# Kernel optimization log

Hardware: AMD Instinct MI355X
Metric: run time of the kernel (lower is better)

## Reference

```python
import jax, jax.numpy as jnp
import numpy as np

N, M = 100000, 12
A, E = 128, 64
BN_EPS = 1e-5

def batchnorm(x, gamma, beta):
    # training-mode BN over leading dim, biased variance (torch default)
    mean = jnp.mean(x, axis=0)
    var = jnp.var(x, axis=0)
    return (x - mean) * jax.lax.rsqrt(var + BN_EPS) * gamma + beta

def setup_inputs() -> dict:
    key = jax.random.key(0)
    ks = jax.random.split(key, 9)
    s_in = 1.0 / np.sqrt(2 * A + E)
    s_skip = 1.0 / np.sqrt(A)
    return {
        "atom_in_fea": jax.random.normal(ks[0], (N, A), jnp.float32),
        "nbr_fea": jax.random.normal(ks[1], (N, M, E), jnp.float32),
        "nbr_fea_idx": jax.random.randint(ks[2], (N, M), 0, N),
        "W_full": jax.random.uniform(ks[3], (2 * A + E, 2 * A), jnp.float32, -s_in, s_in),
        "b_full": jax.random.uniform(ks[4], (2 * A,), jnp.float32, -s_in, s_in),
        "gamma1": jnp.ones((2 * A,), jnp.float32),
        "beta1": jnp.zeros((2 * A,), jnp.float32),
        "gamma2": jnp.ones((A,), jnp.float32),
        "beta2": jnp.zeros((A,), jnp.float32),
        "W_skip": jax.random.uniform(ks[5], (A, A), jnp.float32, -s_skip, s_skip),
        "b_skip": jax.random.uniform(ks[6], (A,), jnp.float32, -s_skip, s_skip),
    }

def reference(atom_in_fea, nbr_fea, nbr_fea_idx, W_full, b_full,
              gamma1, beta1, gamma2, beta2, W_skip, b_skip):
    atom_nbr_fea = atom_in_fea[nbr_fea_idx]                      # [N,M,A] gather
    atom_self_fea = jnp.broadcast_to(atom_in_fea[:, None, :], (N, M, A))
    total = jnp.concatenate([atom_self_fea, atom_nbr_fea, nbr_fea], axis=2)  # [N,M,2A+E]
    gated = jnp.einsum('nmf,fg->nmg', total, W_full) + b_full    # [N,M,2A]
    gated = batchnorm(gated.reshape(-1, 2 * A), gamma1, beta1).reshape(N, M, 2 * A)
    nbr_filter, nbr_core = gated[..., :A], gated[..., A:]
    nbr_sumed = jnp.sum(jax.nn.sigmoid(nbr_filter) * jax.nn.softplus(nbr_core), axis=1)  # [N,A]
    nbr_sumed = batchnorm(nbr_sumed, gamma2, beta2)
    skip_val = atom_in_fea @ W_skip + b_skip
    return jax.nn.softplus(skip_val + nbr_sumed)
```

## Files before the change

### kernel.cpp

```cpp
#include <hip/hip_runtime.h>
#include <stdint.h>

#define N_ATOM 100000
#define M_NBR 12
#define A_FEA 128
#define E_FEA 64
#define KDIM 320
#define GDIM 256
#define ROWS (N_ATOM*M_NBR)
#define BN_EPS 1e-5f

typedef unsigned short u16;
typedef unsigned int u32;
typedef __attribute__((ext_vector_type(8))) short short8;
typedef __attribute__((ext_vector_type(4))) float f32x4;

#define S_BN1SUM 0
#define S_BN1SSQ 256
#define S_S1 512
#define S_T1 768
#define S_BN2SUM 1024
#define S_BN2SSQ 1152
#define S_S2 1280
#define S_T2 1408
#define STATS_F32 1536

#define WPQ_OFF 0
#define W3T_OFF 131072
#define WSK_OFF 163840
#define STATS_OFF 196608
#define P_OFF 202752
#define PQ_BYTES ((size_t)N_ATOM*256*2)
#define Q_OFF (P_OFF + PQ_BYTES)
#define NEED_FAST3 (P_OFF + 2*PQ_BYTES)

__device__ __forceinline__ u16 f2bf(float x) {
    union { float f; u32 u; } v; v.f = x;
    u32 r = v.u + 0x7FFFu + ((v.u >> 16) & 1u);
    return (u16)(r >> 16);
}
__device__ __forceinline__ float bflo(u32 x) { return __uint_as_float(x << 16); }
__device__ __forceinline__ float bfhi(u32 x) { return __uint_as_float(x & 0xFFFF0000u); }
__device__ __forceinline__ float softplus_f(float x) {
    return fmaxf(x, 0.f) + __logf(1.f + __expf(-fabsf(x)));
}
__device__ __forceinline__ float sigmoid_f(float x) {
    return 1.f / (1.f + __expf(-x));
}

__global__ void zero_stats(float* __restrict__ stats) {
    int t = threadIdx.x;
    stats[t] = 0.f;
    stats[256 + t] = 0.f;
    stats[1024 + t] = 0.f;
}

__global__ void finalize1(const float* __restrict__ g1, const float* __restrict__ b1,
                          float* __restrict__ stats) {
    int c = threadIdx.x;
    const float inv_cnt = 1.f / (float)ROWS;
    float mean = stats[S_BN1SUM + c] * inv_cnt;
    float var  = stats[S_BN1SSQ + c] * inv_cnt - mean * mean;
    float iv = rsqrtf(var + BN_EPS);
    float s = g1[c] * iv;
    stats[S_S1 + c] = s;
    stats[S_T1 + c] = fmaf(-mean, s, b1[c]);
}

__global__ void finalize2(const float* __restrict__ g2, const float* __restrict__ b2,
                          float* __restrict__ stats) {
    int c = threadIdx.x;
    const float inv_cnt = 1.f / (float)N_ATOM;
    float mean = stats[S_BN2SUM + c] * inv_cnt;
    float var  = stats[S_BN2SSQ + c] * inv_cnt - mean * mean;
    float iv = rsqrtf(var + BN_EPS);
    float s = g2[c] * iv;
    stats[S_S2 + c] = s;
    stats[S_T2 + c] = fmaf(-mean, s, b2[c]);
}

__global__ void prep_pack2(const float* __restrict__ Wfull,
                           const float* __restrict__ Wskip,
                           u16* __restrict__ wpq, u16* __restrict__ w3t,
                           u16* __restrict__ wsk) {
    int tid = blockIdx.x * blockDim.x + threadIdx.x;
    int l = tid & 63, fr = l & 15, fq = l >> 4;
    if (tid < 8192) {
        int ct = (tid >> 6) & 31;
        int kt = tid >> 11;
        int c = ct * 16 + fr;
        int k0 = kt * 32 + fq * 8;
        u16 tmp[8];
        #pragma unroll
        for (int i = 0; i < 8; ++i) {
            int kk = k0 + i;
            float v = (c < 256) ? Wfull[kk * GDIM + c]
                                : Wfull[(128 + kk) * GDIM + (c - 256)];
            tmp[i] = f2bf(v);
        }
        uint4 pk;
        pk.x = (u32)tmp[0] | ((u32)tmp[1] << 16);
        pk.y = (u32)tmp[2] | ((u32)tmp[3] << 16);
        pk.z = (u32)tmp[4] | ((u32)tmp[5] << 16);
        pk.w = (u32)tmp[6] | ((u32)tmp[7] << 16);
        *reinterpret_cast<uint4*>(&wpq[tid * 8]) = pk;
    } else if (tid < 10240) {
        int t2 = tid - 8192;
        int frag = t2 >> 6;
        int rt16 = frag & 15, kt = frag >> 4;
        int gcol = rt16 * 16 + fr;
        int k0 = kt * 32 + fq * 8;
        u16 tmp[8];
        #pragma unroll
        for (int i = 0; i < 8; ++i) tmp[i] = f2bf(Wfull[(256 + k0 + i) * GDIM + gcol]);
        uint4 pk;
        pk.x = (u32)tmp[0] | ((u32)tmp[1] << 16);
        pk.y = (u32)tmp[2] | ((u32)tmp[3] << 16);
        pk.z = (u32)tmp[4] | ((u32)tmp[5] << 16);
        pk.w = (u32)tmp[6] | ((u32)tmp[7] << 16);
        *reinterpret_cast<uint4*>(&w3t[t2 * 8]) = pk;
    } else if (tid < 12288) {
        int t3 = tid - 10240;
        int ct = (t3 >> 6) & 7;
        int kt = t3 >> 9;
        int c = ct * 16 + fr;
        int k0 = kt * 32 + fq * 8;
        u16 tmp[8];
        #pragma unroll
        for (int i = 0; i < 8; ++i) tmp[i] = f2bf(Wskip[(k0 + i) * A_FEA + c]);
        uint4 pk;
        pk.x = (u32)tmp[0] | ((u32)tmp[1] << 16);
        pk.y = (u32)tmp[2] | ((u32)tmp[3] << 16);
        pk.z = (u32)tmp[4] | ((u32)tmp[5] << 16);
        pk.w = (u32)tmp[6] | ((u32)tmp[7] << 16);
        *reinterpret_cast<uint4*>(&wsk[t3 * 8]) = pk;
    }
}

__launch_bounds__(256)
__global__ void pq_kernel(const float* __restrict__ atom_in,
                          const u16* __restrict__ wpq,
                          u16* __restrict__ Pb, u16* __restrict__ Qb) {
    __shared__ u16 al[64 * 130];
    const int t = threadIdx.x;
    const int w = t >> 6, l = t & 63, fr = l & 15, fq = l >> 4;
    const int n0 = blockIdx.x * 64;

    #pragma unroll
    for (int it = 0; it < 4; ++it) {
        int c = t + it * 256;
        int row = c >> 4, seg = c & 15;
        int n = n0 + row;
        uint4 pk = {0u, 0u, 0u, 0u};
        if (n < N_ATOM) {
            const float* src = atom_in + (size_t)n * A_FEA + seg * 8;
            float4 x0 = *reinterpret_cast<const float4*>(src);
            float4 x1 = *reinterpret_cast<const float4*>(src + 4);
            pk.x = (u32)f2bf(x0.x) | ((u32)f2bf(x0.y) << 16);
            pk.y = (u32)f2bf(x0.z) | ((u32)f2bf(x0.w) << 16);
            pk.z = (u32)f2bf(x1.x) | ((u32)f2bf(x1.y) << 16);
            pk.w = (u32)f2bf(x1.z) | ((u32)f2bf(x1.w) << 16);
        }
        *reinterpret_cast<uint4*>(&al[row * 130 + seg * 8]) = pk;
    }
    __syncthreads();

    f32x4 acc[4][8];
    #pragma unroll
    for (int rt = 0; rt < 4; ++rt)
        #pragma unroll
        for (int p = 0; p < 8; ++p)
            acc[rt][p] = (f32x4){0.f,0.f,0.f,0.f};

    for (int kt = 0; kt < 4; ++kt) {
        short8 af[4], bf[8];
        #pragma unroll
        for (int rt = 0; rt < 4; ++rt)
            af[rt] = *reinterpret_cast<const short8*>(
                &al[(rt * 16 + fr) * 130 + kt * 32 + fq * 8]);
        #pragma unroll
        for (int p = 0; p < 8; ++p)
            bf[p] = *reinterpret_cast<const short8*>(
                &wpq[((kt * 32 + w * 8 + p) * 64 + l) * 8]);
        #pragma unroll
        for (int rt = 0; rt < 4; ++rt)
            #pragma unroll
            for (int p = 0; p < 8; ++p)
                acc[rt][p] = __builtin_amdgcn_mfma_f32_16x16x32_bf16(
                    af[rt], bf[p], acc[rt][p], 0, 0, 0);
    }

    #pragma unroll
    for (int p = 0; p < 8; ++p) {
        int col = w * 128 + p * 16 + fr;
        u16* dst = (col < 256) ? Pb : Qb;
        int cc = (col < 256) ? col : (col - 256);
        #pragma unroll
        for (int rt = 0; rt < 4; ++rt)
            #pragma unroll
            for (int j = 0; j < 4; ++j) {
                int n = n0 + rt * 16 + fq * 4 + j;
                if (n < N_ATOM) dst[(size_t)n * 256 + cc] = f2bf(acc[rt][p][j]);
            }
    }
}

#define NTILES_E (ROWS/96)
#define GRID_E 2500
#define EPAD 66
#define PPAD2 264
#define ACT2 132
#define E_SH6 (96*EPAD*2)
#define P_SH6 E_SH6
#define I_SH6 (E_SH6 + 8*PPAD2*2)
#define SH6_M1 17280
#define SH6_M2 (96*ACT2*4)

template<int MODE>
__launch_bounds__(512, 2)
__global__ void estage6(const float* __restrict__ nbr_fea,
                        const int* __restrict__ nbr_idx,
                        const u16* __restrict__ w3t,
                        const u16* __restrict__ Pb,
                        const u16* __restrict__ Qb,
                        float* __restrict__ stats,
                        float* __restrict__ out_ns) {
    constexpr int SHB = (MODE == 1) ? SH6_M1 : SH6_M2;
    __shared__ __align__(16) unsigned char shraw[SHB];
    u16* e_lds = (u16*)shraw;
    u16* p_lds = (u16*)(shraw + P_SH6);
    int* idx_lds = (int*)(shraw + I_SH6);
    float* act = (float*)shraw;
    float* red = (float*)shraw;

    const int t = threadIdx.x;
    const int w = t >> 6, l = t & 63, fr = l & 15, fq = l >> 4;
    const int gbase0 = w * 16 + fq * 4;

    short8 aw[2][2];
    #pragma unroll
    for (int kt = 0; kt < 2; ++kt)
        #pragma unroll
        for (int rt = 0; rt < 2; ++rt)
            aw[kt][rt] = *reinterpret_cast<const short8*>(
                &w3t[(((kt * 16) + w + rt * 8) * 64 + l) * 8]);

    float s1v[2][4], t1v[2][4];
    if (MODE == 2) {
        #pragma unroll
        for (int rt = 0; rt < 2; ++rt)
            #pragma unroll
            for (int j = 0; j < 4; ++j) {
                int col = gbase0 + rt * 128 + j;
                s1v[rt][j] = stats[S_S1 + col];
                t1v[rt][j] = stats[S_T1 + col];
            }
    }
    float ls[2][4] = {{0,0,0,0},{0,0,0,0}}, lq[2][4] = {{0,0,0,0},{0,0,0,0}};
    float bsum = 0.f, bssq = 0.f;

    for (int tile = blockIdx.x; tile < NTILES_E; tile += GRID_E) {
        const int r0 = tile * 96;
        const int n0a = tile * 8;

        __syncthreads();

        #pragma unroll
        for (int i = 0; i < 2; ++i) {
            int o = t + i * 512;
            if (o < 768) {
                int row = o >> 3, seg = o & 7;
                const float* src = nbr_fea + (size_t)(r0 + row) * E_FEA + seg * 8;
                float4 x0 = *reinterpret_cast<const float4*>(src);
                float4 x1 = *reinterpret_cast<const float4*>(src + 4);
                uint4 pk;
                pk.x = (u32)f2bf(x0.x) | ((u32)f2bf(x0.y) << 16);
                pk.y = (u32)f2bf(x0.z) | ((u32)f2bf(x0.w) << 16);
                pk.z = (u32)f2bf(x1.x) | ((u32)f2bf(x1.y) << 16);
                pk.w = (u32)f2bf(x1.z) | ((u32)f2bf(x1.w) << 16);
                *reinterpret_cast<uint4*>(&e_lds[row * EPAD + seg * 8]) = pk;
            }
        }
        if (t < 256) {
            int row = t >> 5, seg = t & 31;
            *reinterpret_cast<uint4*>(&p_lds[row * PPAD2 + seg * 8]) =
                *reinterpret_cast<const uint4*>(&Pb[(size_t)(n0a + row) * 256 + seg * 8]);
        } else if (t >= 416) {
            int e = t - 416;
            idx_lds[e] = nbr_idx[r0 + e];
        }
        __syncthreads();

        uint2 qv0r[6], qv1r[6];
        #pragma unroll
        for (int ct = 0; ct < 6; ++ct) {
            int edge = ct * 16 + fr;
            int jr = idx_lds[edge];
            const u16* qb = Qb + (size_t)jr * 256;
            qv0r[ct] = *reinterpret_cast<const uint2*>(qb + gbase0);
            qv1r[ct] = *reinterpret_cast<const uint2*>(qb + gbase0 + 128);
        }

        f32x4 acc[2][6];
        #pragma unroll
        for (int rt = 0; rt < 2; ++rt)
            #pragma unroll
            for (int ct = 0; ct < 6; ++ct)
                acc[rt][ct] = (f32x4){0.f,0.f,0.f,0.f};
        #pragma unroll
        for (int kt = 0; kt < 2; ++kt) {
            short8 bf[6];
            #pragma unroll
            for (int ct = 0; ct < 6; ++ct)
                bf[ct] = *reinterpret_cast<const short8*>(
                    &e_lds[(ct * 16 + fr) * EPAD + kt * 32 + fq * 8]);
            #pragma unroll
            for (int rt = 0; rt < 2; ++rt)
                #pragma unroll
                for (int ct = 0; ct < 6; ++ct)
                    acc[rt][ct] = __builtin_amdgcn_mfma_f32_16x16x32_bf16(
                        aw[kt][rt], bf[ct], acc[rt][ct], 0, 0, 0);
        }

        if (MODE == 1) {
            #pragma unroll
            for (int ct = 0; ct < 6; ++ct) {
                int edge = ct * 16 + fr;
                int atom = (edge * 171) >> 11;
                uint2 qv0 = qv0r[ct], qv1 = qv1r[ct];
                uint2 pv0 = *reinterpret_cast<const uint2*>(&p_lds[atom * PPAD2 + gbase0]);
                uint2 pv1 = *reinterpret_cast<const uint2*>(&p_lds[atom * PPAD2 + gbase0 + 128]);
                float g;
                g = acc[0][ct][0] + bflo(qv0.x) + bflo(pv0.x); ls[0][0] += g; lq[0][0] = fmaf(g,g,lq[0][0]);
                g = acc[0][ct][1] + bfhi(qv0.x) + bfhi(pv0.x); ls[0][1] += g; lq[0][1] = fmaf(g,g,lq[0][1]);
                g = acc[0][ct][2] + bflo(qv0.y) + bflo(pv0.y); ls[0][2] += g; lq[0][2] = fmaf(g,g,lq[0][2]);
                g = acc[0][ct][3] + bfhi(qv0.y) + bfhi(pv0.y); ls[0][3] += g; lq[0][3] = fmaf(g,g,lq[0][3]);
                g = acc[1][ct][0] + bflo(qv1.x) + bflo(pv1.x); ls[1][0] += g; lq[1][0] = fmaf(g,g,lq[1][0]);
                g = acc[1][ct][1] + bfhi(qv1.x) + bfhi(pv1.x); ls[1][1] += g; lq[1][1] = fmaf(g,g,lq[1][1]);
                g = acc[1][ct][2] + bflo(qv1.y) + bflo(pv1.y); ls[1][2] += g; lq[1][2] = fmaf(g,g,lq[1][2]);
                g = acc[1][ct][3] + bfhi(qv1.y) + bfhi(pv1.y); ls[1][3] += g; lq[1][3] = fmaf(g,g,lq[1][3]);
            }
        } else {
            float ar[6][4];
            #pragma unroll
            for (int ct = 0; ct < 6; ++ct) {
                int edge = ct * 16 + fr;
                int atom = (edge * 171) >> 11;
                uint2 qv0 = qv0r[ct], qv1 = qv1r[ct];
                uint2 pv0 = *reinterpret_cast<const uint2*>(&p_lds[atom * PPAD2 + gbase0]);
                uint2 pv1 = *reinterpret_cast<const uint2*>(&p_lds[atom * PPAD2 + gbase0 + 128]);
                float gf, gc;
                gf = acc[0][ct][0] + bflo(qv0.x) + bflo(pv0.x);
                gc = acc[1][ct][0] + bflo(qv1.x) + bflo(pv1.x);
                ar[ct][0] = sigmoid_f(fmaf(gf, s1v[0][0], t1v[0][0])) * softplus_f(fmaf(gc, s1v[1][0], t1v[1][0]));
                gf = acc[0][ct][1] + bfhi(qv0.x) + bfhi(pv0.x);
                gc = acc[1][ct][1] + bfhi(qv1.x) + bfhi(pv1.x);
                ar[ct][1] = sigmoid_f(fmaf(gf, s1v[0][1], t1v[0][1])) * softplus_f(fmaf(gc, s1v[1][1], t1v[1][1]));
                gf = acc[0][ct][2] + bflo(qv0.y) + bflo(pv0.y);
                gc = acc[1][ct][2] + bflo(qv1.y) + bflo(pv1.y);
                ar[ct][2] = sigmoid_f(fmaf(gf, s1v[0][2], t1v[0][2])) * softplus_f(fmaf(gc, s1v[1][2], t1v[1][2]));
                gf = acc[0][ct][3] + bfhi(qv0.y) + bfhi(pv0.y);
                gc = acc[1][ct][3] + bfhi(qv1.y) + bfhi(pv1.y);
                ar[ct][3] = sigmoid_f(fmaf(gf, s1v[0][3], t1v[0][3])) * softplus_f(fmaf(gc, s1v[1][3], t1v[1][3]));
            }
            __syncthreads();
            #pragma unroll
            for (int ct = 0; ct < 6; ++ct) {
                int edge = ct * 16 + fr;
                float4 f4 = make_float4(ar[ct][0], ar[ct][1], ar[ct][2], ar[ct][3]);
                *reinterpret_cast<float4*>(&act[edge * ACT2 + gbase0]) = f4;
            }
            __syncthreads();
            #pragma unroll
            for (int i = 0; i < 2; ++i) {
                int o = i * 512 + t;
                int a = o >> 7;
                int c = t & 127;
                float S = 0.f;
                #pragma unroll
                for (int mm = 0; mm < 12; ++mm)
                    S += act[(a * 12 + mm) * ACT2 + c];
                out_ns[(size_t)(n0a + a) * A_FEA + c] = S;
                bsum += S;
                bssq = fmaf(S, S, bssq);
            }
        }
    }

    if (MODE == 1) {
        #pragma unroll
        for (int rt = 0; rt < 2; ++rt)
            #pragma unroll
            for (int j = 0; j < 4; ++j) {
                float s = ls[rt][j], q = lq[rt][j];
                s += __shfl_xor(s, 1, 64);  s += __shfl_xor(s, 2, 64);
                s += __shfl_xor(s, 4, 64);  s += __shfl_xor(s, 8, 64);
                q += __shfl_xor(q, 1, 64);  q += __shfl_xor(q, 2, 64);
                q += __shfl_xor(q, 4, 64);  q += __shfl_xor(q, 8, 64);
                if (fr == 0) {
                    int col = gbase0 + rt * 128 + j;
                    atomicAdd(&stats[S_BN1SUM + col], s);
                    atomicAdd(&stats[S_BN1SSQ + col], q);
                }
            }
    } else {
        __syncthreads();
        if (t >= 128) {
            red[(t - 128) * 2]     = bsum;
            red[(t - 128) * 2 + 1] = bssq;
        }
        __syncthreads();
        if (t < 128) {
            bsum += red[t * 2]     + red[(128 + t) * 2]     + red[(256 + t) * 2];
            bssq += red[t * 2 + 1] + red[(128 + t) * 2 + 1] + red[(256 + t) * 2 + 1];
            atomicAdd(&stats[S_BN2SUM + t], bsum);
            atomicAdd(&stats[S_BN2SSQ + t], bssq);
        }
    }
}

#define BM5 64
__launch_bounds__(256, 2)
__global__ void skip_kernel(const float* __restrict__ atom_in,
                            const u16* __restrict__ wsf,
                            const float* __restrict__ b_skip,
                            const float* __restrict__ stats,
                            float* __restrict__ out) {
    __shared__ u16 a5[BM5 * 136];
    const int t = threadIdx.x;
    const int w = t >> 6, l = t & 63, fr = l & 15, fq = l >> 4;
    const int n0 = blockIdx.x * BM5;

    #pragma unroll
    for (int it = 0; it < 4; ++it) {
        int c = t + it * 256;
        int row = c >> 4, seg = c & 15;
        int n = n0 + row;
        uint4 pk = {0u, 0u, 0u, 0u};
        if (n < N_ATOM) {
            const float* src = atom_in + (size_t)n * A_FEA + seg * 8;
            float4 x0 = *reinterpret_cast<const float4*>(src);
            float4 x1 = *reinterpret_cast<const float4*>(src + 4);
            pk.x = (u32)f2bf(x0.x) | ((u32)f2bf(x0.y) << 16);
            pk.y = (u32)f2bf(x0.z) | ((u32)f2bf(x0.w) << 16);
            pk.z = (u32)f2bf(x1.x) | ((u32)f2bf(x1.y) << 16);
            pk.w = (u32)f2bf(x1.z) | ((u32)f2bf(x1.w) << 16);
        }
        *reinterpret_cast<uint4*>(&a5[row * 136 + seg * 8]) = pk;
    }
    __syncthreads();

    f32x4 acc[4][2];
    #pragma unroll
    for (int rt = 0; rt < 4; ++rt) {
        acc[rt][0] = (f32x4){0.f,0.f,0.f,0.f};
        acc[rt][1] = (f32x4){0.f,0.f,0.f,0.f};
    }
    for (int kt = 0; kt < 4; ++kt) {
        short8 af[4], bf[2];
        #pragma unroll
        for (int rt = 0; rt < 4; ++rt)
            af[rt] = *reinterpret_cast<const short8*>(
                &a5[(rt * 16 + fr) * 136 + kt * 32 + fq * 8]);
        #pragma unroll
        for (int p = 0; p < 2; ++p)
            bf[p] = *reinterpret_cast<const short8*>(
                &wsf[((kt * 8 + 2 * w + p) * 64 + l) * 8]);
        #pragma unroll
        for (int rt = 0; rt < 4; ++rt)
            #pragma unroll
            for (int p = 0; p < 2; ++p)
                acc[rt][p] = __builtin_amdgcn_mfma_f32_16x16x32_bf16(
                    af[rt], bf[p], acc[rt][p], 0, 0, 0);
    }

    #pragma unroll
    for (int p = 0; p < 2; ++p) {
        int col = w * 32 + p * 16 + fr;
        float bs = b_skip[col];
        float s2 = stats[S_S2 + col];
        float t2 = stats[S_T2 + col];
        #pragma unroll
        for (int rt = 0; rt < 4; ++rt)
            #pragma unroll
            for (int j = 0; j < 4; ++j) {
                int n = n0 + rt * 16 + fq * 4 + j;
                if (n < N_ATOM) {
                    size_t o = (size_t)n * A_FEA + col;
                    float S = out[o];
                    out[o] = softplus_f(acc[rt][p][j] + bs + fmaf(S, s2, t2));
                }
            }
    }
}

#define BM 96
#define NTILES (ROWS/BM)
#define GRID_P 2500
#define TPB 256
#define APAD 328
#define ACTPAD 132

__global__ void prep_pack_slow(const float* __restrict__ Wfull,
                               const float* __restrict__ Wskip,
                               u16* __restrict__ wf, u16* __restrict__ wsf) {
    int tid = blockIdx.x * blockDim.x + threadIdx.x;
    if (tid < 10240) {
        int l = tid & 63;
        int ct = (tid >> 6) & 15;
        int kt = tid >> 10;
        int fr = l & 15, fq = l >> 4;
        int col = ct * 16 + fr;
        int k0 = kt * 32 + fq * 8;
        u16 tmp[8];
        #pragma unroll
        for (int i = 0; i < 8; ++i) tmp[i] = f2bf(Wfull[(k0 + i) * GDIM + col]);
        uint4 pk;
        pk.x = (u32)tmp[0] | ((u32)tmp[1] << 16);
        pk.y = (u32)tmp[2] | ((u32)tmp[3] << 16);
        pk.z = (u32)tmp[4] | ((u32)tmp[5] << 16);
        pk.w = (u32)tmp[6] | ((u32)tmp[7] << 16);
        *reinterpret_cast<uint4*>(&wf[tid * 8]) = pk;
    } else if (tid < 12288) {
        int t2 = tid - 10240;
        int l = t2 & 63;
        int ct = (t2 >> 6) & 7;
        int kt = t2 >> 9;
        int fr = l & 15, fq = l >> 4;
        int col = ct * 16 + fr;
        int k0 = kt * 32 + fq * 8;
        u16 tmp[8];
        #pragma unroll
        for (int i = 0; i < 8; ++i) tmp[i] = f2bf(Wskip[(k0 + i) * A_FEA + col]);
        uint4 pk;
        pk.x = (u32)tmp[0] | ((u32)tmp[1] << 16);
        pk.y = (u32)tmp[2] | ((u32)tmp[3] << 16);
        pk.z = (u32)tmp[4] | ((u32)tmp[5] << 16);
        pk.w = (u32)tmp[6] | ((u32)tmp[7] << 16);
        *reinterpret_cast<uint4*>(&wsf[t2 * 8]) = pk;
    }
}

template<int PASS>
__launch_bounds__(TPB, 2)
__global__ void pass_kernel(const float* __restrict__ atom_in,
                            const float* __restrict__ nbr_fea,
                            const int* __restrict__ nbr_idx,
                            const u16* __restrict__ wf,
                            float* __restrict__ stats,
                            float* __restrict__ out_ns) {
    __shared__ union {
        u16 a[BM * APAD];
        float act[BM * ACTPAD];
    } sh;

    const int t = threadIdx.x;
    const int w = t >> 6, l = t & 63, fr = l & 15, fq = l >> 4;
    const int ct0 = 2 * w;

    int colp[4];
    colp[0] = ct0 * 16 + fr;
    colp[1] = colp[0] + 16;
    colp[2] = colp[0] + 128;
    colp[3] = colp[1] + 128;

    float s1v[4], t1v[4];
    if (PASS == 2) {
        #pragma unroll
        for (int p = 0; p < 4; ++p) {
            s1v[p] = stats[S_S1 + colp[p]];
            t1v[p] = stats[S_T1 + colp[p]];
        }
    }
    float ls[4] = {0.f,0.f,0.f,0.f}, lq[4] = {0.f,0.f,0.f,0.f};
    float bsum = 0.f, bssq = 0.f;

    for (int tile = blockIdx.x; tile < NTILES; tile += GRID_P) {
        const int n0 = tile * 8;

        __syncthreads();
        for (int it = 0; it < 15; ++it) {
            int c = t + it * TPB;
            int row = c / 40;
            int seg = c - row * 40;
            int an = row / 12;
            int m  = row - an * 12;
            int na = n0 + an;
            const float* src;
            if (seg < 16) {
                src = atom_in + (size_t)na * A_FEA + seg * 8;
            } else if (seg < 32) {
                int j = nbr_idx[na * M_NBR + m];
                src = atom_in + (size_t)j * A_FEA + (seg - 16) * 8;
            } else {
                src = nbr_fea + ((size_t)na * M_NBR + m) * E_FEA + (seg - 32) * 8;
            }
            float4 x0 = *reinterpret_cast<const float4*>(src);
            float4 x1 = *reinterpret_cast<const float4*>(src + 4);
            uint4 pk;
            pk.x = (u32)f2bf(x0.x) | ((u32)f2bf(x0.y) << 16);
            pk.y = (u32)f2bf(x0.z) | ((u32)f2bf(x0.w) << 16);
            pk.z = (u32)f2bf(x1.x) | ((u32)f2bf(x1.y) << 16);
            pk.w = (u32)f2bf(x1.z) | ((u32)f2bf(x1.w) << 16);
            *reinterpret_cast<uint4*>(&sh.a[row * APAD + seg * 8]) = pk;
        }
        __syncthreads();

        f32x4 acc[6][4];
        #pragma unroll
        for (int rt = 0; rt < 6; ++rt)
            #pragma unroll
            for (int p = 0; p < 4; ++p)
                acc[rt][p] = (f32x4){0.f,0.f,0.f,0.f};

        for (int kt = 0; kt < 10; ++kt) {
            short8 af[6], bf[4];
            #pragma unroll
            for (int rt = 0; rt < 6; ++rt)
                af[rt] = *reinterpret_cast<const short8*>(
                    &sh.a[(rt * 16 + fr) * APAD + kt * 32 + fq * 8]);
            #pragma unroll
            for (int p = 0; p < 4; ++p) {
                int ct = (p < 2) ? (ct0 + p) : (ct0 + 8 + (p - 2));
                bf[p] = *reinterpret_cast<const short8*>(
                    &wf[((kt * 16 + ct) * 64 + l) * 8]);
            }
            #pragma unroll
            for (int rt = 0; rt < 6; ++rt)
                #pragma unroll
                for (int p = 0; p < 4; ++p)
                    acc[rt][p] = __builtin_amdgcn_mfma_f32_16x16x32_bf16(
                        af[rt], bf[p], acc[rt][p], 0, 0, 0);
        }

        if (PASS == 1) {
            #pragma unroll
            for (int p = 0; p < 4; ++p)
                #pragma unroll
                for (int rt = 0; rt < 6; ++rt)
                    #pragma unroll
                    for (int j = 0; j < 4; ++j) {
                        float v = acc[rt][p][j];
                        ls[p] += v;
                        lq[p] = fmaf(v, v, lq[p]);
                    }
        } else {
            __syncthreads();
            #pragma unroll
            for (int rt = 0; rt < 6; ++rt)
                #pragma unroll
                for (int p = 0; p < 2; ++p)
                    #pragma unroll
                    for (int j = 0; j < 4; ++j) {
                        float gf = fmaf(acc[rt][p][j],     s1v[p],     t1v[p]);
                        float gc = fmaf(acc[rt][2 + p][j], s1v[2 + p], t1v[2 + p]);
                        float a = sigmoid_f(gf) * softplus_f(gc);
                        int row = rt * 16 + fq * 4 + j;
                        int colact = ct0 * 16 + p * 16 + fr;
                        sh.act[row * ACTPAD + colact] = a;
                    }
            __syncthreads();
            #pragma unroll
            for (int i = 0; i < 4; ++i) {
                int o = i * TPB + t;
                int a = o >> 7;
                int c = o & 127;
                float S = 0.f;
                #pragma unroll
                for (int mm = 0; mm < 12; ++mm)
                    S += sh.act[(a * 12 + mm) * ACTPAD + c];
                out_ns[(size_t)(n0 + a) * A_FEA + c] = S;
                bsum += S;
                bssq = fmaf(S, S, bssq);
            }
        }
    }

    if (PASS == 1) {
        #pragma unroll
        for (int p = 0; p < 4; ++p) {
            float s = ls[p], q = lq[p];
            s += __shfl_xor(s, 16, 64);
            s += __shfl_xor(s, 32, 64);
            q += __shfl_xor(q, 16, 64);
            q += __shfl_xor(q, 32, 64);
            if (fq == 0) {
                atomicAdd(&stats[S_BN1SUM + colp[p]], s);
                atomicAdd(&stats[S_BN1SSQ + colp[p]], q);
            }
        }
    } else {
        __syncthreads();
        if (t >= 128) {
            sh.act[(t - 128) * 2]     = bsum;
            sh.act[(t - 128) * 2 + 1] = bssq;
        }
        __syncthreads();
        if (t < 128) {
            bsum += sh.act[t * 2];
            bssq += sh.act[t * 2 + 1];
            atomicAdd(&stats[S_BN2SUM + t], bsum);
            atomicAdd(&stats[S_BN2SSQ + t], bssq);
        }
    }
}

extern "C" void kernel_launch(void* const* d_in, const int* in_sizes, int n_in,
                              void* d_out, int out_size, void* d_ws, size_t ws_size,
                              hipStream_t stream) {
    (void)in_sizes; (void)n_in; (void)out_size;
    const float* atom_in = (const float*)d_in[0];
    const float* nbr_fea = (const float*)d_in[1];
    const int*   nbr_idx = (const int*)d_in[2];
    const float* Wfull   = (const float*)d_in[3];
    const float* g1      = (const float*)d_in[5];
    const float* b1      = (const float*)d_in[6];
    const float* g2      = (const float*)d_in[7];
    const float* b2      = (const float*)d_in[8];
    const float* Wsk     = (const float*)d_in[9];
    const float* bsk     = (const float*)d_in[10];
    float* out = (float*)d_out;

    float* stats = (float*)((char*)d_ws + STATS_OFF);
    u16* wskf = (u16*)((char*)d_ws + WSK_OFF);

    if (ws_size >= NEED_FAST3) {
        u16* wpq = (u16*)d_ws;
        u16* w3t = (u16*)((char*)d_ws + W3T_OFF);
        u16* Pb  = (u16*)((char*)d_ws + P_OFF);
        u16* Qb  = (u16*)((char*)d_ws + Q_OFF);

        zero_stats<<<1, 256, 0, stream>>>(stats);
        prep_pack2<<<48, 256, 0, stream>>>(Wfull, Wsk, wpq, w3t, wskf);
        pq_kernel<<<(N_ATOM + 63) / 64, 256, 0, stream>>>(atom_in, wpq, Pb, Qb);
        estage6<1><<<GRID_E, 512, 0, stream>>>(nbr_fea, nbr_idx, w3t, Pb, Qb, stats, out);
        finalize1<<<1, 256, 0, stream>>>(g1, b1, stats);
        estage6<2><<<GRID_E, 512, 0, stream>>>(nbr_fea, nbr_idx, w3t, Pb, Qb, stats, out);
        finalize2<<<1, 128, 0, stream>>>(g2, b2, stats);
        skip_kernel<<<(N_ATOM + BM5 - 1) / BM5, 256, 0, stream>>>(atom_in, wskf, bsk, stats, out);
    } else {
        u16* wf = (u16*)d_ws;
        zero_stats<<<1, 256, 0, stream>>>(stats);
        prep_pack_slow<<<48, 256, 0, stream>>>(Wfull, Wsk, wf, wskf);
        pass_kernel<1><<<GRID_P, TPB, 0, stream>>>(atom_in, nbr_fea, nbr_idx, wf, stats, out);
        finalize1<<<1, 256, 0, stream>>>(g1, b1, stats);
        pass_kernel<2><<<GRID_P, TPB, 0, stream>>>(atom_in, nbr_fea, nbr_idx, wf, stats, out);
        finalize2<<<1, 128, 0, stream>>>(g2, b2, stats);
        skip_kernel<<<(N_ATOM + BM5 - 1) / BM5, 256, 0, stream>>>(atom_in, wskf, bsk, stats, out);
    }
}
```

Baseline: 981.2 us.

## Materialize gated activations in bf16 instead of recomputing GEMM in second pass

Replaces the two-pass recompute scheme (running the edge GEMM twice, once for BN1 stats and once for the activation) with a single GEMM pass that writes the pre-BN gated values as bf16 to workspace, followed by a streaming apply kernel that normalizes, applies sigmoid*softplus, sums over neighbors and accumulates BN2 stats. This removes the second nbr_fea read, gather and MFMA pass at the cost of writing and rereading roughly 600 MB of bf16 intermediate. It also adds bf16 rounding of the pre-BN values and needs a larger workspace, falling back to the old path otherwise.

Result: faster. 841.4 us (-14.3%).

```diff
diff --git a/kernel.cpp b/kernel.cpp
--- a/kernel.cpp
+++ b/kernel.cpp
@@ -33,6 +33,9 @@
 #define PQ_BYTES ((size_t)N_ATOM*256*2)
 #define Q_OFF (P_OFF + PQ_BYTES)
 #define NEED_FAST3 (P_OFF + 2*PQ_BYTES)
+#define GATED_OFF NEED_FAST3
+#define GATED_BYTES ((size_t)ROWS*256*2)
+#define NEED_FASTW (GATED_OFF + GATED_BYTES)
 
 __device__ __forceinline__ u16 f2bf(float x) {
     union { float f; u32 u; } v; v.f = x;
@@ -209,10 +212,206 @@
 #define GRID_E 2500
 #define EPAD 66
 #define PPAD2 264
-#define ACT2 132
 #define E_SH6 (96*EPAD*2)
 #define P_SH6 E_SH6
 #define I_SH6 (E_SH6 + 8*PPAD2*2)
+#define SH7 17280
+
+__launch_bounds__(512, 2)
+__global__ void estage7(const float* __restrict__ nbr_fea,
+                        const int* __restrict__ nbr_idx,
+                        const u16* __restrict__ w3t,
+                        const u16* __restrict__ Pb,
+                        const u16* __restrict__ Qb,
+                        float* __restrict__ stats,
+                        u16* __restrict__ gated) {
+    __shared__ __align__(16) unsigned char shraw[SH7];
+    u16* e_lds = (u16*)shraw;
+    u16* p_lds = (u16*)(shraw + P_SH6);
+    int* idx_lds = (int*)(shraw + I_SH6);
+
+    const int t = threadIdx.x;
+    const int w = t >> 6, l = t & 63, fr = l & 15, fq = l >> 4;
+    const int gbase0 = w * 16 + fq * 4;
+
+    short8 aw[2][2];
+    #pragma unroll
+    for (int kt = 0; kt < 2; ++kt)
+        #pragma unroll
+        for (int rt = 0; rt < 2; ++rt)
+            aw[kt][rt] = *reinterpret_cast<const short8*>(
+                &w3t[(((kt * 16) + w + rt * 8) * 64 + l) * 8]);
+
+    float ls[2][4] = {{0,0,0,0},{0,0,0,0}}, lq[2][4] = {{0,0,0,0},{0,0,0,0}};
+
+    for (int tile = blockIdx.x; tile < NTILES_E; tile += GRID_E) {
+        const int r0 = tile * 96;
+        const int n0a = tile * 8;
+
+        __syncthreads();
+
+        #pragma unroll
+        for (int i = 0; i < 2; ++i) {
+            int o = t + i * 512;
+            if (o < 768) {
+                int row = o >> 3, seg = o & 7;
+                const float* src = nbr_fea + (size_t)(r0 + row) * E_FEA + seg * 8;
+                float4 x0 = *reinterpret_cast<const float4*>(src);
+                float4 x1 = *reinterpret_cast<const float4*>(src + 4);
+                uint4 pk;
+                pk.x = (u32)f2bf(x0.x) | ((u32)f2bf(x0.y) << 16);
+                pk.y = (u32)f2bf(x0.z) | ((u32)f2bf(x0.w) << 16);
+                pk.z = (u32)f2bf(x1.x) | ((u32)f2bf(x1.y) << 16);
+                pk.w = (u32)f2bf(x1.z) | ((u32)f2bf(x1.w) << 16);
+                *reinterpret_cast<uint4*>(&e_lds[row * EPAD + seg * 8]) = pk;
+            }
+        }
+        if (t < 256) {
+            int row = t >> 5, seg = t & 31;
+            *reinterpret_cast<uint4*>(&p_lds[row * PPAD2 + seg * 8]) =
+                *reinterpret_cast<const uint4*>(&Pb[(size_t)(n0a + row) * 256 + seg * 8]);
+        } else if (t >= 416) {
+            int e = t - 416;
+            idx_lds[e] = nbr_idx[r0 + e];
+        }
+        __syncthreads();
+
+        uint2 qv0r[6], qv1r[6];
+        #pragma unroll
+        for (int ct = 0; ct < 6; ++ct) {
+            int edge = ct * 16 + fr;
+            int jr = idx_lds[edge];
+            const u16* qb = Qb + (size_t)jr * 256;
+            qv0r[ct] = *reinterpret_cast<const uint2*>(qb + gbase0);
+            qv1r[ct] = *reinterpret_cast<const uint2*>(qb + gbase0 + 128);
+        }
+
+        f32x4 acc[2][6];
+        #pragma unroll
+        for (int rt = 0; rt < 2; ++rt)
+            #pragma unroll
+            for (int ct = 0; ct < 6; ++ct)
+                acc[rt][ct] = (f32x4){0.f,0.f,0.f,0.f};
+        #pragma unroll
+        for (int kt = 0; kt < 2; ++kt) {
+            short8 bf[6];
+            #pragma unroll
+            for (int ct = 0; ct < 6; ++ct)
+                bf[ct] = *reinterpret_cast<const short8*>(
+                    &e_lds[(ct * 16 + fr) * EPAD + kt * 32 + fq * 8]);
+            #pragma unroll
+            for (int rt = 0; rt < 2; ++rt)
+                #pragma unroll
+                for (int ct = 0; ct < 6; ++ct)
+                    acc[rt][ct] = __builtin_amdgcn_mfma_f32_16x16x32_bf16(
+                        aw[kt][rt], bf[ct], acc[rt][ct], 0, 0, 0);
+        }
+
+        #pragma unroll
+        for (int ct = 0; ct < 6; ++ct) {
+            int edge = ct * 16 + fr;
+            int atom = (edge * 171) >> 11;
+            uint2 qv0 = qv0r[ct], qv1 = qv1r[ct];
+            uint2 pv0 = *reinterpret_cast<const uint2*>(&p_lds[atom * PPAD2 + gbase0]);
+            uint2 pv1 = *reinterpret_cast<const uint2*>(&p_lds[atom * PPAD2 + gbase0 + 128]);
+            float g00 = acc[0][ct][0] + bflo(qv0.x) + bflo(pv0.x);
+            float g01 = acc[0][ct][1] + bfhi(qv0.x) + bfhi(pv0.x);
+            float g02 = acc[0][ct][2] + bflo(qv0.y) + bflo(pv0.y);
+            float g03 = acc[0][ct][3] + bfhi(qv0.y) + bfhi(pv0.y);
+            float g10 = acc[1][ct][0] + bflo(qv1.x) + bflo(pv1.x);
+            float g11 = acc[1][ct][1] + bfhi(qv1.x) + bfhi(pv1.x);
+            float g12 = acc[1][ct][2] + bflo(qv1.y) + bflo(pv1.y);
+            float g13 = acc[1][ct][3] + bfhi(qv1.y) + bfhi(pv1.y);
+            ls[0][0] += g00; lq[0][0] = fmaf(g00,g00,lq[0][0]);
+            ls[0][1] += g01; lq[0][1] = fmaf(g01,g01,lq[0][1]);
+            ls[0][2] += g02; lq[0][2] = fmaf(g02,g02,lq[0][2]);
+            ls[0][3] += g03; lq[0][3] = fmaf(g03,g03,lq[0][3]);
+            ls[1][0] += g10; lq[1][0] = fmaf(g10,g10,lq[1][0]);
+            ls[1][1] += g11; lq[1][1] = fmaf(g11,g11,lq[1][1]);
+            ls[1][2] += g12; lq[1][2] = fmaf(g12,g12,lq[1][2]);
+            ls[1][3] += g13; lq[1][3] = fmaf(g13,g13,lq[1][3]);
+            size_t grow = (size_t)(r0 + edge) * 256;
+            uint2 w0, w1;
+            w0.x = (u32)f2bf(g00) | ((u32)f2bf(g01) << 16);
+            w0.y = (u32)f2bf(g02) | ((u32)f2bf(g03) << 16);
+            w1.x = (u32)f2bf(g10) | ((u32)f2bf(g11) << 16);
+            w1.y = (u32)f2bf(g12) | ((u32)f2bf(g13) << 16);
+            *reinterpret_cast<uint2*>(&gated[grow + gbase0]) = w0;
+            *reinterpret_cast<uint2*>(&gated[grow + gbase0 + 128]) = w1;
+        }
+    }
+
+    #pragma unroll
+    for (int rt = 0; rt < 2; ++rt)
+        #pragma unroll
+        for (int j = 0; j < 4; ++j) {
+            float s = ls[rt][j], q = lq[rt][j];
+            s += __shfl_xor(s, 1, 64);  s += __shfl_xor(s, 2, 64);
+            s += __shfl_xor(s, 4, 64);  s += __shfl_xor(s, 8, 64);
+            q += __shfl_xor(q, 1, 64);  q += __shfl_xor(q, 2, 64);
+            q += __shfl_xor(q, 4, 64);  q += __shfl_xor(q, 8, 64);
+            if (fr == 0) {
+                int col = gbase0 + rt * 128 + j;
+                atomicAdd(&stats[S_BN1SUM + col], s);
+                atomicAdd(&stats[S_BN1SSQ + col], q);
+            }
+        }
+}
+
+__launch_bounds__(256)
+__global__ void apply_kernel(const u16* __restrict__ gated,
+                             float* __restrict__ stats,
+                             float* __restrict__ out) {
+    __shared__ float red[4][64][4];
+    const int t = threadIdx.x;
+    const int lidc = t & 63, aoff = t >> 6;
+    const int c0 = lidc * 2;
+    const int n0 = blockIdx.x * 64;
+
+    const float s1f0 = stats[S_S1 + c0],     t1f0 = stats[S_T1 + c0];
+    const float s1f1 = stats[S_S1 + c0 + 1], t1f1 = stats[S_T1 + c0 + 1];
+    const float s1c0 = stats[S_S1 + 128 + c0],     t1c0 = stats[S_T1 + 128 + c0];
+    const float s1c1 = stats[S_S1 + 128 + c0 + 1], t1c1 = stats[S_T1 + 128 + c0 + 1];
+
+    float bs0 = 0.f, bq0 = 0.f, bs1 = 0.f, bq1 = 0.f;
+
+    for (int a = aoff; a < 64; a += 4) {
+        int n = n0 + a;
+        if (n >= N_ATOM) continue;
+        float S0 = 0.f, S1 = 0.f;
+        const u16* base = gated + (size_t)n * 12 * 256;
+        #pragma unroll
+        for (int m = 0; m < 12; ++m) {
+            u32 uf = *reinterpret_cast<const u32*>(base + m * 256 + c0);
+            u32 uc = *reinterpret_cast<const u32*>(base + m * 256 + 128 + c0);
+            float f0 = bflo(uf), f1 = bfhi(uf);
+            float c_0 = bflo(uc), c_1 = bfhi(uc);
+            float gf0 = fmaf(f0, s1f0, t1f0), gf1 = fmaf(f1, s1f1, t1f1);
+            float gc0 = fmaf(c_0, s1c0, t1c0), gc1 = fmaf(c_1, s1c1, t1c1);
+            S0 += sigmoid_f(gf0) * softplus_f(gc0);
+            S1 += sigmoid_f(gf1) * softplus_f(gc1);
+        }
+        *reinterpret_cast<float2*>(&out[(size_t)n * A_FEA + c0]) = make_float2(S0, S1);
+        bs0 += S0; bq0 = fmaf(S0, S0, bq0);
+        bs1 += S1; bq1 = fmaf(S1, S1, bq1);
+    }
+
+    red[aoff][lidc][0] = bs0; red[aoff][lidc][1] = bq0;
+    red[aoff][lidc][2] = bs1; red[aoff][lidc][3] = bq1;
+    __syncthreads();
+    if (t < 64) {
+        float a0 = red[0][t][0] + red[1][t][0] + red[2][t][0] + red[3][t][0];
+        float a1 = red[0][t][1] + red[1][t][1] + red[2][t][1] + red[3][t][1];
+        float a2 = red[0][t][2] + red[1][t][2] + red[2][t][2] + red[3][t][2];
+        float a3 = red[0][t][3] + red[1][t][3] + red[2][t][3] + red[3][t][3];
+        atomicAdd(&stats[S_BN2SUM + 2 * t],     a0);
+        atomicAdd(&stats[S_BN2SSQ + 2 * t],     a1);
+        atomicAdd(&stats[S_BN2SUM + 2 * t + 1], a2);
+        atomicAdd(&stats[S_BN2SSQ + 2 * t + 1], a3);
+    }
+}
+
+#define ACT2 132
 #define SH6_M1 17280
 #define SH6_M2 (96*ACT2*4)
 
@@ -724,7 +923,22 @@
     float* stats = (float*)((char*)d_ws + STATS_OFF);
     u16* wskf = (u16*)((char*)d_ws + WSK_OFF);
 
-    if (ws_size >= NEED_FAST3) {
+    if (ws_size >= NEED_FASTW) {
+        u16* wpq = (u16*)d_ws;
+        u16* w3t = (u16*)((char*)d_ws + W3T_OFF);
+        u16* Pb  = (u16*)((char*)d_ws + P_OFF);
+        u16* Qb  = (u16*)((char*)d_ws + Q_OFF);
+        u16* gated = (u16*)((char*)d_ws + GATED_OFF);
+
+        zero_stats<<<1, 256, 0, stream>>>(stats);
+        prep_pack2<<<48, 256, 0, stream>>>(Wfull, Wsk, wpq, w3t, wskf);
+        pq_kernel<<<(N_ATOM + 63) / 64, 256, 0, stream>>>(atom_in, wpq, Pb, Qb);
+        estage7<<<GRID_E, 512, 0, stream>>>(nbr_fea, nbr_idx, w3t, Pb, Qb, stats, gated);
+        finalize1<<<1, 256, 0, stream>>>(g1, b1, stats);
+        apply_kernel<<<(N_ATOM + 63) / 64, 256, 0, stream>>>(gated, stats, out);
+        finalize2<<<1, 128, 0, stream>>>(g2, b2, stats);
+        skip_kernel<<<(N_ATOM + BM5 - 1) / BM5, 256, 0, stream>>>(atom_in, wskf, bsk, stats, out);
+    } else if (ws_size >= NEED_FAST3) {
         u16* wpq = (u16*)d_ws;
         u16* w3t = (u16*)((char*)d_ws + W3T_OFF);
         u16* Pb  = (u16*)((char*)d_ws + P_OFF);
```
